# Performance work log

Hardware: AMD Instinct MI355X
Metric: run time of the kernel (lower is better)

Reference implementation:

```python
import jax, jax.numpy as jnp
import numpy as np

NUM_TASKS, IN_SIZE, OUT_SIZE, N_ROWS = 64, 512, 512, 2048


def setup_inputs() -> dict:
    key = jax.random.key(0)
    k_x, k_t, k_w = jax.random.split(key, 3)
    inputs = jax.random.normal(k_x, (N_ROWS, IN_SIZE), dtype=jnp.float32)
    task_ids = jax.random.randint(k_t, (N_ROWS,), 0, NUM_TASKS, dtype=jnp.int64)
    # in_size == out_size path: identity + N(0, 0.03) perturbation per task
    W = (jnp.eye(IN_SIZE, OUT_SIZE, dtype=jnp.float32)[None]
         + 0.03 * jax.random.normal(k_w, (NUM_TASKS, IN_SIZE, OUT_SIZE), dtype=jnp.float32))
    return {"inputs": inputs, "task_ids": task_ids, "W": W}


def reference(inputs, task_ids, W):
    # Gather the full per-row weight matrix then batched vector-matrix multiply,
    # faithful to torch.einsum('ni,nio->no', inputs, W[task_ids]).
    aligned = W[task_ids]                       # [I, in, out]
    return jnp.einsum("ni,nio->no", inputs, aligned)  # [I, out]
```

## Files before the change

kernel.cpp:

```cpp
#include <hip/hip_runtime.h>


#define KDIM   512
#define NDIM   512
#define NCOL   64
#define GROWS  64
#define TSTR   40

typedef _Float16 __attribute__((ext_vector_type(8))) f16x8;
typedef _Float16 __attribute__((ext_vector_type(4))) f16x4;
typedef float    __attribute__((ext_vector_type(4))) f32x4;

__global__ __launch_bounds__(256) void tsl_mfma(
    const float* __restrict__ x,
    const int*   __restrict__ tids,
    const float* __restrict__ W,
    float*       __restrict__ out,
    int n_rows)
{
    const int tid  = threadIdx.x;
    const int lane = tid & 63;
    const int wv   = tid >> 6;
    const int task = blockIdx.y;
    const int c0   = blockIdx.x * NCOL;

    __shared__ unsigned short rowlist[2048];
    __shared__ __align__(16) char smem[40960];

    _Float16* Wt = (_Float16*)(smem + wv * 10240);
    _Float16* xs = (_Float16*)(smem + wv * 10240 + 5120);
    float*    red = (float*)smem;

    int count = 0;
    for (int base = 0; base < n_rows; base += 64) {
        const int row = base + lane;
        const bool m = (row < n_rows) && (tids[row] == task);
        const unsigned long long bal = __ballot(m);
        const int rank = __popcll(bal & ((1ull << lane) - 1ull));
        if (wv == 0 && m) rowlist[count + rank] = (unsigned short)row;
        count += __popcll(bal);
    }
    __syncthreads();
    if (count == 0) return;

    const int ml = lane & 15;
    const int q  = lane >> 4;
    const float* Wg = W + (size_t)task * KDIM * NDIM + c0;
    const int kw = wv * 128;

    for (int g0 = 0; g0 < count; g0 += GROWS) {
        f32x4 acc[4][4] = {};

        #pragma unroll
        for (int kt = 0; kt < 4; ++kt) {
            const int k0 = kw + kt * 32;

            #pragma unroll
            for (int p = 0; p < 2; ++p) {
                const int kb = p * 16 + q * 4;
                const float* gp = Wg + (size_t)(k0 + kb) * NDIM + ml * 4;
                const float4 r0 = *(const float4*)(gp);
                const float4 r1 = *(const float4*)(gp + NDIM);
                const float4 r2 = *(const float4*)(gp + 2 * NDIM);
                const float4 r3 = *(const float4*)(gp + 3 * NDIM);
                _Float16* wp = Wt + (ml * 4) * TSTR + kb;
                f16x4 v0 = {(_Float16)r0.x, (_Float16)r1.x, (_Float16)r2.x, (_Float16)r3.x};
                f16x4 v1 = {(_Float16)r0.y, (_Float16)r1.y, (_Float16)r2.y, (_Float16)r3.y};
                f16x4 v2 = {(_Float16)r0.z, (_Float16)r1.z, (_Float16)r2.z, (_Float16)r3.z};
                f16x4 v3 = {(_Float16)r0.w, (_Float16)r1.w, (_Float16)r2.w, (_Float16)r3.w};
                *(f16x4*)(wp)             = v0;
                *(f16x4*)(wp + TSTR)      = v1;
                *(f16x4*)(wp + 2 * TSTR)  = v2;
                *(f16x4*)(wp + 3 * TSTR)  = v3;
            }

            #pragma unroll
            for (int u = 0; u < 8; ++u) {
                const int r  = u * 8 + (lane >> 3);
                const int kq = (lane & 7) * 4;
                const int rr = g0 + r;
                const int row = rowlist[(rr < count) ? rr : g0];
                const float4 v = *(const float4*)(x + (size_t)row * KDIM + k0 + kq);
                f16x4 h = {(_Float16)v.x, (_Float16)v.y, (_Float16)v.z, (_Float16)v.w};
                *(f16x4*)(xs + r * TSTR + kq) = h;
            }

            f16x8 af[4], bf[4];
            #pragma unroll
            for (int rt = 0; rt < 4; ++rt)
                af[rt] = *(const f16x8*)(xs + (rt * 16 + ml) * TSTR + q * 8);
            #pragma unroll
            for (int ct = 0; ct < 4; ++ct)
                bf[ct] = *(const f16x8*)(Wt + (ct * 16 + ml) * TSTR + q * 8);
            #pragma unroll
            for (int rt = 0; rt < 4; ++rt)
                #pragma unroll
                for (int ct = 0; ct < 4; ++ct)
                    acc[rt][ct] = __builtin_amdgcn_mfma_f32_16x16x32_f16(
                        af[rt], bf[ct], acc[rt][ct], 0, 0, 0);
        }

        #pragma unroll
        for (int h = 0; h < 2; ++h) {
            __syncthreads();
            #pragma unroll
            for (int rt2 = 0; rt2 < 2; ++rt2) {
                const int rt = h * 2 + rt2;
                #pragma unroll
                for (int ct = 0; ct < 4; ++ct)
                    #pragma unroll
                    for (int rg = 0; rg < 4; ++rg) {
                        const int row = rt2 * 16 + q * 4 + rg;
                        const int col = ct * 16 + ml;
                        red[wv * 2048 + row * 64 + col] = acc[rt][ct][rg];
                    }
            }
            __syncthreads();
            #pragma unroll
            for (int t2 = 0; t2 < 2; ++t2) {
                const int idx = t2 * 1024 + tid * 4;
                const float4 a0 = *(const float4*)&red[idx];
                const float4 a1 = *(const float4*)&red[2048 + idx];
                const float4 a2 = *(const float4*)&red[4096 + idx];
                const float4 a3 = *(const float4*)&red[6144 + idx];
                float4 s;
                s.x = a0.x + a1.x + a2.x + a3.x;
                s.y = a0.y + a1.y + a2.y + a3.y;
                s.z = a0.z + a1.z + a2.z + a3.z;
                s.w = a0.w + a1.w + a2.w + a3.w;
                const int r  = h * 32 + (idx >> 6);
                const int c  = idx & 63;
                const int rr = g0 + r;
                if (rr < count)
                    *(float4*)(out + (size_t)rowlist[rr] * NDIM + c0 + c) = s;
            }
        }
        __syncthreads();
    }
}

extern "C" void kernel_launch(void* const* d_in, const int* in_sizes, int n_in,
                              void* d_out, int out_size, void* d_ws, size_t ws_size,
                              hipStream_t stream) {
    const float* x    = (const float*)d_in[0];
    const int*   tids = (const int*)d_in[1];
    const float* W    = (const float*)d_in[2];
    float*       out  = (float*)d_out;
    const int n_rows  = in_sizes[1];

    dim3 grid(NDIM / NCOL, 64);
    dim3 block(256);
    tsl_mfma<<<grid, block, 0, stream>>>(x, tids, W, out, n_rows);
}
```

Measured before the change: 116.1 us.

## Split K across blocks with separate row-bucketing and reduction kernels

Bucketing rows by task moves out of every GEMM block, which each used to rescan all task ids, into one atomic-based bucketing kernel. The GEMM grid gains a K-split dimension of 4, so there are four times as many blocks, each doing one 32-wide K step per wave. Partial sums go to a workspace buffer and a final kernel adds the four slices. This adds two extra launches, a memset, and extra global traffic for the partials (about 16 MB written and read) in exchange for more parallelism and shorter per-block work. The order of rows within each task's list now depends on atomics, and rows only reach the partial buffer if their task count is nonzero.

```diff
diff --git a/kernel.cpp b/kernel.cpp
--- a/kernel.cpp
+++ b/kernel.cpp
@@ -1,104 +1,110 @@
 #include <hip/hip_runtime.h>
 
 
-#define KDIM   512
-#define NDIM   512
-#define NCOL   64
-#define GROWS  64
-#define TSTR   40
+#define KDIM  512
+#define NDIM  512
+#define TSTR  40
 
-typedef _Float16 __attribute__((ext_vector_type(8))) f16x8;
-typedef _Float16 __attribute__((ext_vector_type(4))) f16x4;
-typedef float    __attribute__((ext_vector_type(4))) f32x4;
+typedef _Float16 f16x8 __attribute__((ext_vector_type(8)));
+typedef _Float16 f16x4 __attribute__((ext_vector_type(4)));
+typedef float    f32x4 __attribute__((ext_vector_type(4)));
 
-__global__ __launch_bounds__(256) void tsl_mfma(
-    const float* __restrict__ x,
-    const int*   __restrict__ tids,
-    const float* __restrict__ W,
-    float*       __restrict__ out,
-    int n_rows)
+__global__ __launch_bounds__(256) void k_rowlist(
+    const int* __restrict__ tids, int* __restrict__ cnt,
+    int* __restrict__ rows, int n_rows)
+{
+    const int i = blockIdx.x * 256 + threadIdx.x;
+    if (i < n_rows) {
+        const int t = tids[i];
+        const int p = atomicAdd(&cnt[t], 1);
+        rows[t * 2048 + p] = i;
+    }
+}
+
+__global__ __launch_bounds__(256) void k_gemm(
+    const float* __restrict__ x, const float* __restrict__ W,
+    const int* __restrict__ cnt, const int* __restrict__ rows,
+    float* __restrict__ part)
 {
     const int tid  = threadIdx.x;
     const int lane = tid & 63;
     const int wv   = tid >> 6;
+    const int c0   = blockIdx.x * 64;
     const int task = blockIdx.y;
-    const int c0   = blockIdx.x * NCOL;
+    const int ks   = blockIdx.z;
 
-    __shared__ unsigned short rowlist[2048];
+    const int count = cnt[task];
+    if (count == 0) return;
+
+    const int k0 = ks * 128 + wv * 32;
+
     __shared__ __align__(16) char smem[40960];
-
-    _Float16* Wt = (_Float16*)(smem + wv * 10240);
-    _Float16* xs = (_Float16*)(smem + wv * 10240 + 5120);
+    _Float16* Wt  = (_Float16*)(smem + wv * 10240);
+    _Float16* xs  = (_Float16*)(smem + wv * 10240 + 5120);
     float*    red = (float*)smem;
-
-    int count = 0;
-    for (int base = 0; base < n_rows; base += 64) {
-        const int row = base + lane;
-        const bool m = (row < n_rows) && (tids[row] == task);
-        const unsigned long long bal = __ballot(m);
-        const int rank = __popcll(bal & ((1ull << lane) - 1ull));
-        if (wv == 0 && m) rowlist[count + rank] = (unsigned short)row;
-        count += __popcll(bal);
-    }
-    __syncthreads();
-    if (count == 0) return;
 
     const int ml = lane & 15;
     const int q  = lane >> 4;
     const float* Wg = W + (size_t)task * KDIM * NDIM + c0;
-    const int kw = wv * 128;
+    const int*   rl = rows + task * 2048;
+    float*       pb = part + (size_t)ks * 2048 * NDIM;
 
-    for (int g0 = 0; g0 < count; g0 += GROWS) {
-        f32x4 acc[4][4] = {};
+    for (int g0 = 0; g0 < count; g0 += 64) {
+        int rowv[8];
+        #pragma unroll
+        for (int u = 0; u < 8; ++u) {
+            const int rr = g0 + u * 8 + (lane >> 3);
+            rowv[u] = rl[(rr < count) ? rr : g0];
+        }
+        float4 xv[8];
+        #pragma unroll
+        for (int u = 0; u < 8; ++u)
+            xv[u] = *(const float4*)(x + (size_t)rowv[u] * KDIM + k0 + (lane & 7) * 4);
+
+        const int ko = q * 8;
+        float4 wr[8];
+        #pragma unroll
+        for (int j = 0; j < 8; ++j)
+            wr[j] = *(const float4*)(Wg + (size_t)(k0 + ko + j) * NDIM + ml * 4);
 
         #pragma unroll
-        for (int kt = 0; kt < 4; ++kt) {
-            const int k0 = kw + kt * 32;
+        for (int u = 0; u < 8; ++u) {
+            const int r = u * 8 + (lane >> 3);
+            f16x4 h = {(_Float16)xv[u].x, (_Float16)xv[u].y,
+                       (_Float16)xv[u].z, (_Float16)xv[u].w};
+            *(f16x4*)(xs + r * TSTR + (lane & 7) * 4) = h;
+        }
+        {
+            f16x8 h0 = {(_Float16)wr[0].x, (_Float16)wr[1].x, (_Float16)wr[2].x, (_Float16)wr[3].x,
+                        (_Float16)wr[4].x, (_Float16)wr[5].x, (_Float16)wr[6].x, (_Float16)wr[7].x};
+            f16x8 h1 = {(_Float16)wr[0].y, (_Float16)wr[1].y, (_Float16)wr[2].y, (_Float16)wr[3].y,
+                        (_Float16)wr[4].y, (_Float16)wr[5].y, (_Float16)wr[6].y, (_Float16)wr[7].y};
+            f16x8 h2 = {(_Float16)wr[0].z, (_Float16)wr[1].z, (_Float16)wr[2].z, (_Float16)wr[3].z,
+                        (_Float16)wr[4].z, (_Float16)wr[5].z, (_Float16)wr[6].z, (_Float16)wr[7].z};
+            f16x8 h3 = {(_Float16)wr[0].w, (_Float16)wr[1].w, (_Float16)wr[2].w, (_Float16)wr[3].w,
+                        (_Float16)wr[4].w, (_Float16)wr[5].w, (_Float16)wr[6].w, (_Float16)wr[7].w};
+            _Float16* wp = Wt + (ml * 4) * TSTR + ko;
+            *(f16x8*)(wp)            = h0;
+            *(f16x8*)(wp + TSTR)     = h1;
+            *(f16x8*)(wp + 2 * TSTR) = h2;
+            *(f16x8*)(wp + 3 * TSTR) = h3;
+        }
 
-            #pragma unroll
-            for (int p = 0; p < 2; ++p) {
-                const int kb = p * 16 + q * 4;
-                const float* gp = Wg + (size_t)(k0 + kb) * NDIM + ml * 4;
-                const float4 r0 = *(const float4*)(gp);
-                const float4 r1 = *(const float4*)(gp + NDIM);
-                const float4 r2 = *(const float4*)(gp + 2 * NDIM);
-                const float4 r3 = *(const float4*)(gp + 3 * NDIM);
-                _Float16* wp = Wt + (ml * 4) * TSTR + kb;
-                f16x4 v0 = {(_Float16)r0.x, (_Float16)r1.x, (_Float16)r2.x, (_Float16)r3.x};
-                f16x4 v1 = {(_Float16)r0.y, (_Float16)r1.y, (_Float16)r2.y, (_Float16)r3.y};
-                f16x4 v2 = {(_Float16)r0.z, (_Float16)r1.z, (_Float16)r2.z, (_Float16)r3.z};
-                f16x4 v3 = {(_Float16)r0.w, (_Float16)r1.w, (_Float16)r2.w, (_Float16)r3.w};
-                *(f16x4*)(wp)             = v0;
-                *(f16x4*)(wp + TSTR)      = v1;
-                *(f16x4*)(wp + 2 * TSTR)  = v2;
-                *(f16x4*)(wp + 3 * TSTR)  = v3;
-            }
+        f16x8 af[4], bf[4];
+        #pragma unroll
+        for (int rt = 0; rt < 4; ++rt)
+            af[rt] = *(const f16x8*)(xs + (rt * 16 + ml) * TSTR + q * 8);
+        #pragma unroll
+        for (int ct = 0; ct < 4; ++ct)
+            bf[ct] = *(const f16x8*)(Wt + (ct * 16 + ml) * TSTR + q * 8);
 
-            #pragma unroll
-            for (int u = 0; u < 8; ++u) {
-                const int r  = u * 8 + (lane >> 3);
-                const int kq = (lane & 7) * 4;
-                const int rr = g0 + r;
-                const int row = rowlist[(rr < count) ? rr : g0];
-                const float4 v = *(const float4*)(x + (size_t)row * KDIM + k0 + kq);
-                f16x4 h = {(_Float16)v.x, (_Float16)v.y, (_Float16)v.z, (_Float16)v.w};
-                *(f16x4*)(xs + r * TSTR + kq) = h;
-            }
-
-            f16x8 af[4], bf[4];
-            #pragma unroll
-            for (int rt = 0; rt < 4; ++rt)
-                af[rt] = *(const f16x8*)(xs + (rt * 16 + ml) * TSTR + q * 8);
+        f32x4 acc[4][4] = {};
+        #pragma unroll
+        for (int rt = 0; rt < 4; ++rt)
             #pragma unroll
             for (int ct = 0; ct < 4; ++ct)
-                bf[ct] = *(const f16x8*)(Wt + (ct * 16 + ml) * TSTR + q * 8);
-            #pragma unroll
-            for (int rt = 0; rt < 4; ++rt)
-                #pragma unroll
-                for (int ct = 0; ct < 4; ++ct)
-                    acc[rt][ct] = __builtin_amdgcn_mfma_f32_16x16x32_f16(
-                        af[rt], bf[ct], acc[rt][ct], 0, 0, 0);
-        }
+                acc[rt][ct] = __builtin_amdgcn_mfma_f32_16x16x32_f16(
+                    af[rt], bf[ct], acc[rt][ct], 0, 0, 0);
 
         #pragma unroll
         for (int h = 0; h < 2; ++h) {
@@ -109,11 +115,9 @@
                 #pragma unroll
                 for (int ct = 0; ct < 4; ++ct)
                     #pragma unroll
-                    for (int rg = 0; rg < 4; ++rg) {
-                        const int row = rt2 * 16 + q * 4 + rg;
-                        const int col = ct * 16 + ml;
-                        red[wv * 2048 + row * 64 + col] = acc[rt][ct][rg];
-                    }
+                    for (int rg = 0; rg < 4; ++rg)
+                        red[wv * 2048 + (rt2 * 16 + q * 4 + rg) * 64 + ct * 16 + ml]
+                            = acc[rt][ct][rg];
             }
             __syncthreads();
             #pragma unroll
@@ -132,11 +136,24 @@
                 const int c  = idx & 63;
                 const int rr = g0 + r;
                 if (rr < count)
-                    *(float4*)(out + (size_t)rowlist[rr] * NDIM + c0 + c) = s;
+                    *(float4*)(pb + (size_t)rl[rr] * NDIM + c0 + c) = s;
             }
         }
         __syncthreads();
     }
+}
+
+__global__ __launch_bounds__(256) void k_reduce(
+    const float* __restrict__ part, float* __restrict__ out)
+{
+    const int i = blockIdx.x * 256 + threadIdx.x;
+    const f32x4* p = (const f32x4*)part;
+    const f32x4 a = p[i];
+    const f32x4 b = p[262144 + i];
+    const f32x4 c = p[524288 + i];
+    const f32x4 d = p[786432 + i];
+    f32x4 s = a + b + c + d;
+    ((f32x4*)out)[i] = s;
 }
 
 extern "C" void kernel_launch(void* const* d_in, const int* in_sizes, int n_in,
@@ -148,7 +165,12 @@
     float*       out  = (float*)d_out;
     const int n_rows  = in_sizes[1];
 
-    dim3 grid(NDIM / NCOL, 64);
-    dim3 block(256);
-    tsl_mfma<<<grid, block, 0, stream>>>(x, tids, W, out, n_rows);
+    int*   cnt  = (int*)d_ws;
+    int*   rows = (int*)d_ws + 64;
+    float* part = (float*)((char*)d_ws + (1 << 20));
+
+    hipMemsetAsync(cnt, 0, 64 * sizeof(int), stream);
+    k_rowlist<<<dim3((n_rows + 255) / 256), dim3(256), 0, stream>>>(tids, cnt, rows, n_rows);
+    k_gemm<<<dim3(8, 64, 4), dim3(256), 0, stream>>>(x, W, cnt, rows, part);
+    k_reduce<<<dim3(2048 * 512 / 4 / 256), dim3(256), 0, stream>>>(part, out);
 }
```

Measured after the change: 116.5 us. No clear change (+0.3%).
